# Optimization experiments

Hardware: AMD Instinct MI355X
Metric: run time of the kernel (lower is better)

## Reference

```python
import jax, jax.numpy as jnp
import numpy as np

EPS = 1e-6


def _mp_match(reps, att, kernel):
    """BiMPM multi-perspective match.
    reps: (B,L,D); att: (B,L,D) or (B,1,D); kernel: (M,D).
    Returns (B,L,1+M): [tanh(sum(reps*att)), tanh(sum_d reps*kernel_m*att)].
    """
    prod = reps * att                                   # (B,L,D)
    cos = jnp.tanh(jnp.sum(prod, axis=-1, keepdims=True))   # (B,L,1)
    mp = jnp.tanh(jnp.einsum('bld,md->blm', prod, kernel))  # (B,L,M)
    return jnp.concatenate([cos, mp], axis=-1)


def setup_inputs() -> dict:
    key = jax.random.key(0)
    ks = jax.random.split(key, 12)
    B, Llt, Lrt, D, M, A = 32, 128, 128, 512, 64, 128
    H = D // 2
    u = lambda k, shape: jax.random.uniform(k, shape, jnp.float32, -0.05, 0.05)  # keras 'uniform' init
    return {
        'reps_lt': jax.random.normal(ks[0], (B, Llt, D), jnp.float32),
        'h_lt_fw': jax.random.normal(ks[1], (B, H), jnp.float32),
        'h_lt_bw': jax.random.normal(ks[2], (B, H), jnp.float32),
        'reps_rt': jax.random.normal(ks[3], (B, Lrt, D), jnp.float32),
        'h_rt_fw': jax.random.normal(ks[4], (B, H), jnp.float32),
        'h_rt_bw': jax.random.normal(ks[5], (B, H), jnp.float32),
        'kernel_full': u(ks[6], (M, D)),
        'kernel_mpool': u(ks[7], (M, D)),
        'attn_w1': u(ks[8], (D, A)),
        'diag_w': u(ks[9], (A,)),
        'kernel_att': u(ks[10], (M, D)),
        'kernel_maxatt': u(ks[11], (M, D)),
    }


def reference(reps_lt, h_lt_fw, h_lt_bw, reps_rt, h_rt_fw, h_rt_bw,
              kernel_full, kernel_mpool, attn_w1, diag_w,
              kernel_att, kernel_maxatt):
    # ---- full match: each left timestep vs last BiLSTM state of right ----
    h_rt = jnp.concatenate([h_rt_fw, h_rt_bw], axis=-1)[:, None, :]  # (B,1,D)
    full = _mp_match(reps_lt, h_rt, kernel_full)                     # (B,Ll,1+M)

    # ---- max-pooling match ----
    # t[b,r,l,m] = tanh(sum_d R[b,r,d]*K[m,d]*L[b,l,d]); max over right positions r
    r_scaled = jnp.einsum('brd,md->brmd', reps_rt, kernel_mpool)     # (B,Lr,M,D)
    t = jnp.tanh(jnp.einsum('brmd,bld->brlm', r_scaled, reps_lt))    # (B,Lr,Ll,M)
    mpool = jnp.max(t, axis=1)                                       # (B,Ll,M)

    # ---- attentive match ----
    a_lt = jnp.tanh(reps_lt @ attn_w1) * diag_w                      # (B,Ll,A)
    a_rt = jnp.tanh(reps_rt @ attn_w1)                               # (B,Lr,A)
    scores = jnp.einsum('bla,bra->blr', a_lt, a_rt)                  # (B,Ll,Lr)
    probs = jax.nn.softmax(scores, axis=-1)
    att = jnp.einsum('blr,brd->bld', probs, reps_rt)                 # (B,Ll,D)
    attentive = _mp_match(reps_lt, att, kernel_att)                  # (B,Ll,1+M)

    # ---- max-attentive match ----
    num = jnp.einsum('bld,brd->blr', reps_lt, reps_rt)
    n_lt = jnp.sqrt(jnp.maximum(jnp.sum(reps_lt * reps_lt, -1), EPS))[:, :, None]
    n_rt = jnp.sqrt(jnp.maximum(jnp.sum(reps_rt * reps_rt, -1), EPS))[:, None, :]
    rel = num / n_rt / n_lt                                          # (B,Ll,Lr)
    idx = jnp.argmax(rel, axis=2)                                    # (B,Ll) int
    max_att = jnp.take_along_axis(reps_rt, idx[:, :, None], axis=1)  # (B,Ll,D)
    maxatt = _mp_match(reps_lt, max_att, kernel_maxatt)              # (B,Ll,1+M)

    return jnp.concatenate([full, mpool, attentive, maxatt], axis=-1)  # (B,Ll,3+4M)
```

## Files before the change

kernel.cpp:

```cpp
#include <hip/hip_runtime.h>
#include <hip/hip_bf16.h>
#include <math.h>
#include <stdint.h>

typedef __attribute__((ext_vector_type(8))) short short8;
typedef __attribute__((ext_vector_type(4))) float float4v;

#define DEV static __device__ __forceinline__

DEV float bflo(unsigned int u) { union { unsigned int i; float f; } v; v.i = u << 16; return v.f; }
DEV float bfhi(unsigned int u) { union { unsigned int i; float f; } v; v.i = u & 0xffff0000u; return v.f; }
DEV unsigned short f2bf(float f) {
    union { float f; unsigned int i; } v; v.f = f;
    unsigned int x = v.i;
    return (unsigned short)((x + 0x7fffu + ((x >> 16) & 1u)) >> 16);
}
DEV unsigned int pack2(float a, float b) { return (unsigned int)f2bf(a) | ((unsigned int)f2bf(b) << 16); }
#if __has_builtin(__builtin_amdgcn_cvt_pk_bf16_f32)
DEV unsigned int pack2_fast(float a, float b) {
    typedef __attribute__((ext_vector_type(2))) short short2v;
    short2v r = __builtin_amdgcn_cvt_pk_bf16_f32(a, b);
    union { short2v s; unsigned int u; } v; v.s = r; return v.u;
}
#else
DEV unsigned int pack2_fast(float a, float b) { return pack2(a, b); }
#endif
DEV void unpack8(uint4 u, float* f) {
    f[0]=bflo(u.x); f[1]=bfhi(u.x); f[2]=bflo(u.y); f[3]=bfhi(u.y);
    f[4]=bflo(u.z); f[5]=bfhi(u.z); f[6]=bflo(u.w); f[7]=bfhi(u.w);
}

DEV void async16(const unsigned short* g, unsigned short* l) {
    __builtin_amdgcn_global_load_lds(
        (const __attribute__((address_space(1))) unsigned int*)g,
        (__attribute__((address_space(3))) unsigned int*)l, 16, 0, 0);
}

__global__ __launch_bounds__(256) void prep_kernel(const float* __restrict__ lt,
                                                   const float* __restrict__ rt,
                                                   const float* __restrict__ kf,
                                                   const float* __restrict__ kmp,
                                                   const float* __restrict__ ka,
                                                   const float* __restrict__ km,
                                                   const float* __restrict__ w1,
                                                   unsigned short* __restrict__ ltb,
                                                   unsigned short* __restrict__ rtb,
                                                   unsigned short* __restrict__ kb,
                                                   unsigned short* __restrict__ w1t,
                                                   double* __restrict__ rsq) {
    __shared__ double ws2[2][2];
    __shared__ float tile[32][33];
    int bid = blockIdx.x, t = threadIdx.x;
    if (bid < 1024) {
        bool isRt = bid >= 512;
        int base = (isRt ? (bid - 512) : bid) * 8;
        int rl = t >> 7;
        int c  = t & 127;
        const float* srcb = isRt ? rt : lt;
        unsigned short* dstb = isRt ? rtb : ltb;
        #pragma unroll
        for (int p = 0; p < 4; ++p) {
            int row = base + p * 2 + rl;
            const float* src = srcb + (size_t)row * 512;
            float4 v = *(const float4*)(src + c * 4);
            ushort4 o;
            o.x = f2bf(v.x); o.y = f2bf(v.y); o.z = f2bf(v.z); o.w = f2bf(v.w);
            *(ushort4*)(dstb + (size_t)row * 512 + c * 4) = o;
            if (isRt) {
                double s = (double)v.x * v.x + (double)v.y * v.y
                         + (double)v.z * v.z + (double)v.w * v.w;
                #pragma unroll
                for (int off = 1; off < 64; off <<= 1) s += __shfl_xor(s, off, 64);
                if ((c & 63) == 0) ws2[rl][c >> 6] = s;
                __syncthreads();
                if (c == 0) rsq[row] = 1.0 / sqrt(ws2[rl][0] + ws2[rl][1]);
                __syncthreads();
            }
        }
    } else if (bid < 1152) {
        int kbk = bid - 1024;
        int ksel = kbk >> 5;
        const float* src = (ksel == 0) ? kf : (ksel == 1) ? kmp : (ksel == 2) ? ka : km;
        int off = (kbk & 31) * 1024 + t * 4;
        float4 v = *(const float4*)(src + off);
        ushort4 o;
        o.x = f2bf(v.x); o.y = f2bf(v.y); o.z = f2bf(v.z); o.w = f2bf(v.w);
        *(ushort4*)(kb + ksel * 32768 + off) = o;
    } else {
        int b2 = bid - 1152;
        int d0 = (b2 & 15) * 32, a0 = (b2 >> 4) * 32;
        int r = t >> 5, c = t & 31;
        #pragma unroll
        for (int i = 0; i < 32; i += 8)
            tile[r + i][c] = w1[(size_t)(d0 + r + i) * 128 + a0 + c];
        __syncthreads();
        #pragma unroll
        for (int i = 0; i < 32; i += 8)
            w1t[(size_t)(a0 + r + i) * 512 + d0 + c] = f2bf(tile[c][r + i]);
    }
}

__global__ __launch_bounds__(256, 3) void uber_kernel(
        const unsigned short* __restrict__ ltb,
        const unsigned short* __restrict__ rtb,
        const unsigned short* __restrict__ kmb,
        const unsigned short* __restrict__ w1t,
        const float* __restrict__ diag,
        unsigned short* __restrict__ a_all,
        const float* __restrict__ ltf,
        const float* __restrict__ rtf,
        const double* __restrict__ rsq,
        int* __restrict__ idxout,
        float* __restrict__ out) {
    __shared__ __align__(16) unsigned char smem[52224];
    int bx = blockIdx.x;
    int t = threadIdx.x;
    int wave = t >> 6, lane = t & 63;
    int q = lane >> 4, col = lane & 15, kq = q * 8;

    if (bx < 2048) {
        int xcd = bx & 7, jj = bx >> 3;
        int b = xcd * 4 + (jj >> 6);
        int m = jj & 63;
        unsigned short (*ltS)[72] = (unsigned short(*)[72])smem;
        unsigned short* rtL = (unsigned short*)(smem + 18432);
        float (*mx)[2] = (float(*)[2])(smem + 18432 + 32768);
        int wl = wave & 1, wr = wave >> 1;
        const unsigned short* ltp = ltb + (size_t)b * 65536;
        const unsigned short* rtp = rtb + (size_t)b * 65536;
        const unsigned short* kr = kmb + (size_t)m * 512;
        int srow = t >> 3, cg8 = t & 7, cg = cg8 * 8;
        int gsw = (cg8 ^ (srow & 7)) * 8;
        int wbase = (t & ~63) * 8;

        #pragma unroll
        for (int it = 0; it < 4; ++it)
            async16(rtp + (size_t)(it * 32 + srow) * 512 + gsw,
                    rtL + it * 2048 + wbase);
        uint4 pk = *(const uint4*)(kr + cg);
        uint4 plt[4];
        #pragma unroll
        for (int it = 0; it < 4; ++it)
            plt[it] = *(const uint4*)(ltp + (size_t)(it * 32 + srow) * 512 + cg);

        float4v acc[4][4] = {};
        for (int k0i = 0; k0i < 8; ++k0i) {
            float kf8[8]; unpack8(pk, kf8);
            #pragma unroll
            for (int it = 0; it < 4; ++it) {
                int row = it * 32 + srow;
                float lf[8]; unpack8(plt[it], lf);
                uint4 s;
                s.x = pack2_fast(lf[0] * kf8[0], lf[1] * kf8[1]);
                s.y = pack2_fast(lf[2] * kf8[2], lf[3] * kf8[3]);
                s.z = pack2_fast(lf[4] * kf8[4], lf[5] * kf8[5]);
                s.w = pack2_fast(lf[6] * kf8[6], lf[7] * kf8[7]);
                *(uint4*)&ltS[row][cg] = s;
            }
            __syncthreads();
            if (k0i < 7) {
                int k0n = (k0i + 1) * 64;
                int bofs = ((k0i + 1) & 1) * 8192;
                #pragma unroll
                for (int it = 0; it < 4; ++it)
                    async16(rtp + (size_t)(it * 32 + srow) * 512 + k0n + gsw,
                            rtL + bofs + it * 2048 + wbase);
                pk = *(const uint4*)(kr + k0n + cg);
                #pragma unroll
                for (int it = 0; it < 4; ++it)
                    plt[it] = *(const uint4*)(ltp + (size_t)(it * 32 + srow) * 512 + k0n + cg);
            }
            const unsigned short* rb = rtL + (k0i & 1) * 8192;
            #pragma unroll
            for (int kk = 0; kk < 64; kk += 32) {
                short8 af[4], bfr[4];
                #pragma unroll
                for (int i = 0; i < 4; ++i)
                    af[i] = *(const short8*)&ltS[wl * 64 + i * 16 + col][kk + kq];
                #pragma unroll
                for (int j = 0; j < 4; ++j) {
                    int row = wr * 64 + j * 16 + col;
                    int slot = ((kk >> 3) + q) ^ (row & 7);
                    bfr[j] = *(const short8*)&rb[row * 64 + slot * 8];
                }
                #pragma unroll
                for (int i = 0; i < 4; ++i)
                    #pragma unroll
                    for (int j = 0; j < 4; ++j)
                        acc[i][j] = __builtin_amdgcn_mfma_f32_16x16x32_bf16(af[i], bfr[j], acc[i][j], 0, 0, 0);
            }
            __syncthreads();
        }
        #pragma unroll
        for (int i = 0; i < 4; ++i)
            #pragma unroll
            for (int ii = 0; ii < 4; ++ii) {
                float v = fmaxf(fmaxf(acc[i][0][ii], acc[i][1][ii]), fmaxf(acc[i][2][ii], acc[i][3][ii]));
                #pragma unroll
                for (int off = 1; off < 16; off <<= 1) v = fmaxf(v, __shfl_xor(v, off, 64));
                if (col == 0) mx[wl * 64 + i * 16 + q * 4 + ii][wr] = v;
            }
        __syncthreads();
        if (t < 128)
            out[((size_t)(b * 128 + t)) * 259 + 65 + m] = tanhf(fmaxf(mx[t][0], mx[t][1]));

    } else if (bx < 2560) {
        int idA = bx - 2048;
        int xcd = idA & 7, jj = idA >> 3;
        int b = xcd * 4 + (jj >> 4);
        int L0 = (jj & 15) * 8;
        float* ltS = (float*)smem;
        float* buf = (float*)(smem + 16384);
        double* dvs = (double*)(smem + 49152);
        float* wv1 = (float*)(smem + 49152 + 128);
        float* wv2 = wv1 + 16;
        int* wi1 = (int*)(wv2 + 16);
        int* wi2 = wi1 + 16;
        int* candi = wi2 + 16;
        {
            int row = t >> 5, c0 = (t & 31) * 16;
            const float* src = ltf + ((size_t)(b * 128 + L0 + row)) * 512 + c0;
            #pragma unroll
            for (int i = 0; i < 4; ++i)
                *(float4*)&ltS[row * 512 + c0 + i * 4] = *(const float4*)(src + i * 4);
        }
        int lg = t >> 7;
        int rg = (t >> 2) & 31;
        int ds = t & 3;
        float acc[4][4] = {{0.f}};
        for (int p = 0; p < 8; ++p) {
            __syncthreads();
            {
                int row = t >> 1, c0 = (t & 1) * 32;
                const float* src = rtf + ((size_t)(b * 128 + row)) * 512 + p * 64 + c0;
                float f[32];
                #pragma unroll
                for (int i = 0; i < 8; ++i)
                    *(float4*)&f[i * 4] = *(const float4*)(src + i * 4);
                int base = row * 64;
                #pragma unroll
                for (int gg = 0; gg < 4; ++gg) {
                    int g = (t & 1) * 4 + gg;
                    int o = ((g ^ (row & 7)) * 8);
                    #pragma unroll
                    for (int k = 0; k < 8; ++k) buf[base + o + k] = f[gg * 8 + k];
                }
            }
            __syncthreads();
            #pragma unroll
            for (int sub = 0; sub < 2; ++sub) {
                int dloc = ds * 16 + sub * 8;
                int dglob = p * 64 + dloc;
                float a[4][8];
                #pragma unroll
                for (int i = 0; i < 4; ++i)
                    #pragma unroll
                    for (int k = 0; k < 8; ++k) a[i][k] = ltS[(lg * 4 + i) * 512 + dglob + k];
                int g = dloc >> 3;
                #pragma unroll
                for (int j = 0; j < 4; ++j) {
                    int r = rg + j * 32;
                    const float* rp = &buf[r * 64 + ((g ^ (r & 7)) * 8)];
                    float rv[8];
                    #pragma unroll
                    for (int k = 0; k < 8; ++k) rv[k] = rp[k];
                    #pragma unroll
                    for (int i = 0; i < 4; ++i)
                        #pragma unroll
                        for (int k = 0; k < 8; ++k)
                            acc[i][j] = fmaf(a[i][k], rv[k], acc[i][j]);
                }
            }
        }
        #pragma unroll
        for (int i = 0; i < 4; ++i)
            #pragma unroll
            for (int j = 0; j < 4; ++j) {
                acc[i][j] += __shfl_xor(acc[i][j], 1, 64);
                acc[i][j] += __shfl_xor(acc[i][j], 2, 64);
            }
        float v1[4], v2[4]; int i1[4], i2[4];
        #pragma unroll
        for (int i = 0; i < 4; ++i) {
            v1[i] = -3.0e38f; v2[i] = -3.0e38f; i1[i] = 0; i2[i] = 1;
            #pragma unroll
            for (int j = 0; j < 4; ++j) {
                int r = rg + j * 32;
                float s = acc[i][j] * (float)rsq[b * 128 + r];
                if (s > v1[i]) { v2[i] = v1[i]; i2[i] = i1[i]; v1[i] = s; i1[i] = r; }
                else if (s > v2[i]) { v2[i] = s; i2[i] = r; }
            }
        }
        #pragma unroll
        for (int off = 4; off < 64; off <<= 1) {
            #pragma unroll
            for (int i = 0; i < 4; ++i) {
                float u1 = __shfl_xor(v1[i], off, 64); int j1 = __shfl_xor(i1[i], off, 64);
                float u2 = __shfl_xor(v2[i], off, 64); int j2 = __shfl_xor(i2[i], off, 64);
                if (u1 > v1[i]) {
                    float ov = v1[i]; int oi = i1[i];
                    v1[i] = u1; i1[i] = j1;
                    if (u2 > ov) { v2[i] = u2; i2[i] = j2; } else { v2[i] = ov; i2[i] = oi; }
                } else if (u1 > v2[i]) { v2[i] = u1; i2[i] = j1; }
            }
        }
        if (lane == 0) {
            #pragma unroll
            for (int i = 0; i < 4; ++i) {
                int l = lg * 4 + i, h = wave & 1;
                wv1[l * 2 + h] = v1[i]; wi1[l * 2 + h] = i1[i];
                wv2[l * 2 + h] = v2[i]; wi2[l * 2 + h] = i2[i];
            }
        }
        __syncthreads();
        if (t < 8) {
            float a1 = wv1[t * 2], a2 = wv2[t * 2]; int ai1 = wi1[t * 2], ai2 = wi2[t * 2];
            float b1 = wv1[t * 2 + 1], b2 = wv2[t * 2 + 1]; int bi1 = wi1[t * 2 + 1], bi2 = wi2[t * 2 + 1];
            int ri1, ri2;
            if (b1 > a1) {
                ri1 = bi1;
                if (b2 > a1) { ri2 = bi2; } else { ri2 = ai1; }
            } else {
                ri1 = ai1;
                if (b1 > a2) { ri2 = bi1; } else { ri2 = ai2; }
            }
            candi[t * 2] = ri1; candi[t * 2 + 1] = ri2;
            (void)a2; (void)b2; (void)ai2; (void)bi2;
        }
        __syncthreads();
        {
            int dotid = t >> 4;
            int sub = t & 15;
            int l = dotid >> 1, c = dotid & 1;
            int r = candi[l * 2 + c];
            const float* lrow = ltf + ((size_t)(b * 128 + L0 + l)) * 512;
            const float* rrow = rtf + ((size_t)(b * 128 + r)) * 512;
            double s = 0.0;
            #pragma unroll 8
            for (int k = 0; k < 32; ++k) {
                int d = sub * 32 + k;
                s = fma((double)lrow[d], (double)rrow[d], s);
            }
            #pragma unroll
            for (int off = 1; off < 16; off <<= 1) s += __shfl_xor(s, off, 64);
            if (sub == 0) dvs[l * 2 + c] = s * rsq[b * 128 + r];
        }
        __syncthreads();
        if (t < 8) {
            int ia = candi[t * 2], ib = candi[t * 2 + 1];
            double va = dvs[t * 2], vb = dvs[t * 2 + 1];
            int res = (vb > va || (vb == va && ib < ia)) ? ib : ia;
            idxout[b * 128 + L0 + t] = res;
        }

    } else {
        int R0 = (bx - 2560) * 32;
        unsigned short (*aS)[72] = (unsigned short(*)[72])smem;
        unsigned short (*bS)[72] = (unsigned short(*)[72])(smem + 4608);
        float* diagS = (float*)(smem + 4608 + 18432);
        int wl = wave & 1, wr = wave >> 1;
        if (t < 128) diagS[t] = diag[t];
        const unsigned short* src = (R0 < 4096) ? (ltb + (size_t)R0 * 512) : (rtb + (size_t)(R0 - 4096) * 512);
        float4v acc[4] = {};
        for (int k0 = 0; k0 < 512; k0 += 64) {
            {
                int row = t >> 3, cg = (t & 7) * 8;
                *(uint4*)&aS[row][cg] = *(const uint4*)(src + (size_t)row * 512 + k0 + cg);
            }
            #pragma unroll
            for (int it = 0; it < 4; ++it) {
                int id = it * 256 + t;
                int row = id >> 3, cg = (id & 7) * 8;
                *(uint4*)&bS[row][cg] = *(const uint4*)(w1t + (size_t)row * 512 + k0 + cg);
            }
            __syncthreads();
            #pragma unroll
            for (int kk = 0; kk < 64; kk += 32) {
                short8 af = *(const short8*)&aS[wl * 16 + col][kk + kq];
                #pragma unroll
                for (int j = 0; j < 4; ++j) {
                    short8 bf = *(const short8*)&bS[wr * 64 + j * 16 + col][kk + kq];
                    acc[j] = __builtin_amdgcn_mfma_f32_16x16x32_bf16(af, bf, acc[j], 0, 0, 0);
                }
            }
            __syncthreads();
        }
        bool isLt = (R0 < 4096);
        #pragma unroll
        for (int j = 0; j < 4; ++j)
            #pragma unroll
            for (int ii = 0; ii < 4; ++ii) {
                int rowl = wl * 16 + q * 4 + ii;
                int n = wr * 64 + j * 16 + col;
                float v = tanhf(acc[j][ii]);
                if (isLt) v *= diagS[n];
                a_all[((size_t)(R0 + rowl)) * 128 + n] = f2bf(v);
            }
    }
}

__global__ __launch_bounds__(512, 4) void tail_kernel(
        const unsigned short* __restrict__ a_all,
        const unsigned short* __restrict__ rtb,
        const float* __restrict__ ltf,
        const unsigned short* __restrict__ kb,
        const float* __restrict__ hfw,
        const float* __restrict__ hbw,
        const int* __restrict__ idxp,
        float* __restrict__ out) {
    __shared__ __align__(16) unsigned char smem[81664];
    int bx = blockIdx.x;
    int t = threadIdx.x;
    int wave = t >> 6, lane = t & 63;
    int q = lane >> 4, col = lane & 15, kq = q * 8;

    if (bx < 256) {
        int b = bx & 31, lg = bx >> 5;
        int L0 = lg * 16;
        unsigned short (*altS)[136]  = (unsigned short(*)[136])(smem);
        unsigned short (*artS)[136]  = (unsigned short(*)[136])(smem + 4352);
        unsigned short (*rtS)[512]   = (unsigned short(*)[512])(smem + 39168);
        unsigned short (*prodsF)[520]= (unsigned short(*)[520])(smem + 55552);
        float (*P)[132]  = (float(*)[132])(smem + 72192);
        float (*pmax)[8] = (float(*)[8])(smem + 80640);
        float (*psum)[8] = (float(*)[8])(smem + 81152);
        const unsigned short* kb_att = kb + 2 * 32768;

        if (t < 256) {
            int row = t >> 4, c0 = (t & 15) * 8;
            *(uint4*)&altS[row][c0] = *(const uint4*)(a_all + ((size_t)(b * 128 + L0 + row)) * 128 + c0);
        }
        {
            int row = t >> 2, c0 = (t & 3) * 32;
            const unsigned short* src = a_all + ((size_t)(4096 + b * 128 + row)) * 128 + c0;
            #pragma unroll
            for (int i = 0; i < 4; ++i)
                *(uint4*)&artS[row][c0 + i * 8] = *(const uint4*)(src + i * 8);
        }
        __syncthreads();

        float4v acc = {};
        #pragma unroll
        for (int kk = 0; kk < 128; kk += 32) {
            short8 af = *(const short8*)&altS[col][kk + kq];
            short8 bf = *(const short8*)&artS[wave * 16 + col][kk + kq];
            acc = __builtin_amdgcn_mfma_f32_16x16x32_bf16(af, bf, acc, 0, 0, 0);
        }
        float m4[4], p4[4];
        #pragma unroll
        for (int ii = 0; ii < 4; ++ii) {
            float v = acc[ii];
            #pragma unroll
            for (int off = 1; off < 16; off <<= 1) v = fmaxf(v, __shfl_xor(v, off, 64));
            m4[ii] = v;
        }
        if (col == 0) {
            #pragma unroll
            for (int ii = 0; ii < 4; ++ii) pmax[q * 4 + ii][wave] = m4[ii];
        }
        __syncthreads();
        #pragma unroll
        for (int ii = 0; ii < 4; ++ii) {
            float M = pmax[q * 4 + ii][0];
            #pragma unroll
            for (int w = 1; w < 8; ++w) M = fmaxf(M, pmax[q * 4 + ii][w]);
            p4[ii] = expf(acc[ii] - M);
            float s = p4[ii];
            #pragma unroll
            for (int off = 1; off < 16; off <<= 1) s += __shfl_xor(s, off, 64);
            m4[ii] = s;
        }
        if (col == 0) {
            #pragma unroll
            for (int ii = 0; ii < 4; ++ii) psum[q * 4 + ii][wave] = m4[ii];
        }
        __syncthreads();
        #pragma unroll
        for (int ii = 0; ii < 4; ++ii) {
            float S = psum[q * 4 + ii][0] + psum[q * 4 + ii][1] + psum[q * 4 + ii][2] + psum[q * 4 + ii][3]
                    + psum[q * 4 + ii][4] + psum[q * 4 + ii][5] + psum[q * 4 + ii][6] + psum[q * 4 + ii][7];
            P[q * 4 + ii][wave * 16 + col] = p4[ii] / S;
        }

        int l = t >> 5, cd = t & 31;
        float a8[2][8] = {{0.f}};
        for (int rcb = 0; rcb < 128; rcb += 16) {
            __syncthreads();
            {
                int row = t >> 5, c0 = (t & 31) * 16;
                const unsigned short* src = rtb + ((size_t)(b * 128 + rcb + row)) * 512 + c0;
                *(uint4*)&rtS[row][c0] = *(const uint4*)src;
                *(uint4*)&rtS[row][c0 + 8] = *(const uint4*)(src + 8);
            }
            __syncthreads();
            for (int rr = 0; rr < 16; ++rr) {
                float pr = P[l][rcb + rr];
                #pragma unroll
                for (int pass = 0; pass < 2; ++pass) {
                    uint4 u = *(const uint4*)&rtS[rr][pass * 256 + cd * 8];
                    float f[8]; unpack8(u, f);
                    #pragma unroll
                    for (int k = 0; k < 8; ++k) a8[pass][k] += pr * f[k];
                }
            }
        }

        int grow = b * 128 + L0 + l;
        const float* ltrow = ltf + (size_t)grow * 512;
        float csum = 0.f;
        #pragma unroll
        for (int pass = 0; pass < 2; ++pass) {
            int d0 = pass * 256 + cd * 8;
            float lf[8];
            *(float4*)&lf[0] = *(const float4*)(ltrow + d0);
            *(float4*)&lf[4] = *(const float4*)(ltrow + d0 + 4);
            float pf[8];
            #pragma unroll
            for (int k = 0; k < 8; ++k) { pf[k] = lf[k] * a8[pass][k]; csum += pf[k]; }
            uint4 o;
            o.x = pack2(pf[0], pf[1]); o.y = pack2(pf[2], pf[3]);
            o.z = pack2(pf[4], pf[5]); o.w = pack2(pf[6], pf[7]);
            *(uint4*)&prodsF[l][d0] = o;
        }
        #pragma unroll
        for (int off = 1; off < 32; off <<= 1) csum += __shfl_xor(csum, off, 64);
        if (cd == 0) out[(size_t)grow * 259 + 129] = tanhf(csum);

        unsigned short* Ks = &artS[0][0];
        float* red = (float*)&rtS[0][0];
        for (int half = 0; half < 2; ++half) {
            __syncthreads();
            {
                int row = t >> 4, c0 = (t & 15) * 32;
                const unsigned short* src = kb_att + ((size_t)(half * 32 + row)) * 512 + c0;
                #pragma unroll
                for (int i = 0; i < 4; ++i)
                    *(uint4*)&Ks[row * 520 + c0 + i * 8] = *(const uint4*)(src + i * 8);
            }
            __syncthreads();
            float4v pacc[2] = {};
            #pragma unroll
            for (int kk = 0; kk < 64; kk += 32) {
                short8 af = *(const short8*)&prodsF[col][wave * 64 + kk + kq];
                #pragma unroll
                for (int j = 0; j < 2; ++j) {
                    short8 bf = *(const short8*)&Ks[(j * 16 + col) * 520 + wave * 64 + kk + kq];
                    pacc[j] = __builtin_amdgcn_mfma_f32_16x16x32_bf16(af, bf, pacc[j], 0, 0, 0);
                }
            }
            #pragma unroll
            for (int j = 0; j < 2; ++j)
                #pragma unroll
                for (int ii = 0; ii < 4; ++ii)
                    red[((wave * 2 + j) * 16 + q * 4 + ii) * 16 + col] = pacc[j][ii];
            __syncthreads();
            {
                int ll = t >> 5, jm = t & 31;
                int j = jm >> 4, mc = jm & 15;
                float s = 0.f;
                #pragma unroll
                for (int w = 0; w < 8; ++w) s += red[((w * 2 + j) * 16 + ll) * 16 + mc];
                out[((size_t)(b * 128 + L0 + ll)) * 259 + 130 + half * 32 + jm] = tanhf(s);
            }
        }

    } else {
        int idB = bx - 256;
        int lg = idB & 7, b = (idB >> 3) & 31;
        int mode = (idB >> 8) ? 2 : 0;
        int L0 = lg * 16;
        unsigned short (*prods)[520] = (unsigned short(*)[520])smem;
        unsigned short* Ks = (unsigned short*)(smem + 16640);
        float* red = (float*)(smem + 49920);
        const unsigned short* Kp = kb + (size_t)((mode == 0) ? 0 : 3 * 32768);
        int obase = (mode == 0) ? 0 : 194;

        if (t < 256) {
            int l = t >> 4, c = t & 15;
            int grow = b * 128 + L0 + l;
            const float* ltrow = ltf + (size_t)grow * 512;
            const unsigned short* avrow = 0;
            if (mode == 2) avrow = rtb + ((size_t)(b * 128 + idxp[grow])) * 512;
            float csum = 0.f;
            #pragma unroll
            for (int pass = 0; pass < 4; ++pass) {
                int d0 = pass * 128 + c * 8;
                float lf[8], af[8], pf[8];
                *(float4*)&lf[0] = *(const float4*)(ltrow + d0);
                *(float4*)&lf[4] = *(const float4*)(ltrow + d0 + 4);
                if (mode == 0) {
                    const float* h = (d0 < 256) ? (hfw + b * 256 + d0) : (hbw + b * 256 + d0 - 256);
                    *(float4*)&af[0] = *(const float4*)h;
                    *(float4*)&af[4] = *(const float4*)(h + 4);
                } else {
                    uint4 av = *(const uint4*)(avrow + d0);
                    unpack8(av, af);
                }
                #pragma unroll
                for (int k = 0; k < 8; ++k) { pf[k] = lf[k] * af[k]; csum += pf[k]; }
                uint4 o;
                o.x = pack2(pf[0], pf[1]); o.y = pack2(pf[2], pf[3]);
                o.z = pack2(pf[4], pf[5]); o.w = pack2(pf[6], pf[7]);
                *(uint4*)&prods[l][d0] = o;
            }
            #pragma unroll
            for (int off = 1; off < 16; off <<= 1) csum += __shfl_xor(csum, off, 64);
            if (c == 0) out[(size_t)grow * 259 + obase] = tanhf(csum);
        }
        for (int half = 0; half < 2; ++half) {
            {
                int row = t >> 4, c0 = (t & 15) * 32;
                const unsigned short* src = Kp + ((size_t)(half * 32 + row)) * 512 + c0;
                #pragma unroll
                for (int i = 0; i < 4; ++i)
                    *(uint4*)&Ks[row * 520 + c0 + i * 8] = *(const uint4*)(src + i * 8);
            }
            __syncthreads();
            float4v acc2[2] = {};
            #pragma unroll
            for (int kk = 0; kk < 64; kk += 32) {
                short8 af = *(const short8*)&prods[col][wave * 64 + kk + kq];
                #pragma unroll
                for (int j = 0; j < 2; ++j) {
                    short8 bf = *(const short8*)&Ks[(j * 16 + col) * 520 + wave * 64 + kk + kq];
                    acc2[j] = __builtin_amdgcn_mfma_f32_16x16x32_bf16(af, bf, acc2[j], 0, 0, 0);
                }
            }
            #pragma unroll
            for (int j = 0; j < 2; ++j)
                #pragma unroll
                for (int ii = 0; ii < 4; ++ii)
                    red[((wave * 2 + j) * 16 + q * 4 + ii) * 16 + col] = acc2[j][ii];
            __syncthreads();
            {
                int ll = t >> 5, jm = t & 31;
                int j = jm >> 4, mc = jm & 15;
                float s = 0.f;
                #pragma unroll
                for (int w = 0; w < 8; ++w) s += red[((w * 2 + j) * 16 + ll) * 16 + mc];
                out[((size_t)(b * 128 + L0 + ll)) * 259 + obase + 1 + half * 32 + jm] = tanhf(s);
            }
            __syncthreads();
        }
    }
}

extern "C" void kernel_launch(void* const* d_in, const int* in_sizes, int n_in,
                              void* d_out, int out_size, void* d_ws, size_t ws_size,
                              hipStream_t stream) {
    const float* lt  = (const float*)d_in[0];
    const float* rt  = (const float*)d_in[3];
    const float* hfw = (const float*)d_in[4];
    const float* hbw = (const float*)d_in[5];
    const float* kf  = (const float*)d_in[6];
    const float* kmp = (const float*)d_in[7];
    const float* w1  = (const float*)d_in[8];
    const float* dia = (const float*)d_in[9];
    const float* ka  = (const float*)d_in[10];
    const float* km  = (const float*)d_in[11];
    float* out = (float*)d_out;

    char* wsb = (char*)d_ws;
    unsigned short* ltb16 = (unsigned short*)(wsb);
    unsigned short* rtb16 = (unsigned short*)(wsb + 4194304);
    unsigned short* kb16  = (unsigned short*)(wsb + 8388608);
    unsigned short* w1t   = (unsigned short*)(wsb + 8650752);
    unsigned short* a_all = (unsigned short*)(wsb + 8781824);
    double*         rsq   = (double*)(wsb + 15073280);
    int*            idx   = (int*)(wsb + 15106048);

    prep_kernel<<<1216, 256, 0, stream>>>(lt, rt, kf, kmp, ka, km, w1, ltb16, rtb16, kb16, w1t, rsq);
    uber_kernel<<<2816, 256, 0, stream>>>(ltb16, rtb16, kb16 + 32768, w1t, dia, a_all,
                                          lt, rt, rsq, idx, out);
    tail_kernel<<<768, 512, 0, stream>>>(a_all, rtb16, lt, kb16, hfw, hbw, idx, out);
}
```

Measured before the change: 188.9 us.

## Load max-pool MFMA operands directly from global memory, dropping LDS staging

The max-pooling match block no longer stages the left (kernel-scaled) and right tiles through shared memory with async global-to-LDS copies and double buffering. Each lane now reads its MFMA fragments straight from global memory, scaling the left fragment by the kernel row in registers, and all intra-loop barriers are removed. This cuts LDS traffic and synchronisation but makes each wave re-read operands other waves also use. It depends on L2/cache hits and gives up the explicit prefetch overlap, and the global fragment reads are strided by row.

```diff
diff --git a/kernel.cpp b/kernel.cpp
--- a/kernel.cpp
+++ b/kernel.cpp
@@ -28,12 +28,6 @@
 DEV void unpack8(uint4 u, float* f) {
     f[0]=bflo(u.x); f[1]=bfhi(u.x); f[2]=bflo(u.y); f[3]=bfhi(u.y);
     f[4]=bflo(u.z); f[5]=bfhi(u.z); f[6]=bflo(u.w); f[7]=bfhi(u.w);
-}
-
-DEV void async16(const unsigned short* g, unsigned short* l) {
-    __builtin_amdgcn_global_load_lds(
-        (const __attribute__((address_space(1))) unsigned int*)g,
-        (__attribute__((address_space(3))) unsigned int*)l, 16, 0, 0);
 }
 
 __global__ __launch_bounds__(256) void prep_kernel(const float* __restrict__ lt,
@@ -122,66 +116,38 @@
         int xcd = bx & 7, jj = bx >> 3;
         int b = xcd * 4 + (jj >> 6);
         int m = jj & 63;
-        unsigned short (*ltS)[72] = (unsigned short(*)[72])smem;
-        unsigned short* rtL = (unsigned short*)(smem + 18432);
-        float (*mx)[2] = (float(*)[2])(smem + 18432 + 32768);
+        float (*mx)[2] = (float(*)[2])smem;
         int wl = wave & 1, wr = wave >> 1;
-        const unsigned short* ltp = ltb + (size_t)b * 65536;
-        const unsigned short* rtp = rtb + (size_t)b * 65536;
-        const unsigned short* kr = kmb + (size_t)m * 512;
-        int srow = t >> 3, cg8 = t & 7, cg = cg8 * 8;
-        int gsw = (cg8 ^ (srow & 7)) * 8;
-        int wbase = (t & ~63) * 8;
-
-        #pragma unroll
-        for (int it = 0; it < 4; ++it)
-            async16(rtp + (size_t)(it * 32 + srow) * 512 + gsw,
-                    rtL + it * 2048 + wbase);
-        uint4 pk = *(const uint4*)(kr + cg);
-        uint4 plt[4];
-        #pragma unroll
-        for (int it = 0; it < 4; ++it)
-            plt[it] = *(const uint4*)(ltp + (size_t)(it * 32 + srow) * 512 + cg);
+
+        const unsigned short* pK = kmb + (size_t)m * 512 + kq;
+        const unsigned short* pA[4];
+        const unsigned short* pB[4];
+        #pragma unroll
+        for (int i = 0; i < 4; ++i) {
+            pA[i] = ltb + ((size_t)(b * 128 + wl * 64 + i * 16 + col)) * 512 + kq;
+            pB[i] = rtb + ((size_t)(b * 128 + wr * 64 + i * 16 + col)) * 512 + kq;
+        }
 
         float4v acc[4][4] = {};
+        #pragma unroll
         for (int k0i = 0; k0i < 8; ++k0i) {
-            float kf8[8]; unpack8(pk, kf8);
-            #pragma unroll
-            for (int it = 0; it < 4; ++it) {
-                int row = it * 32 + srow;
-                float lf[8]; unpack8(plt[it], lf);
-                uint4 s;
-                s.x = pack2_fast(lf[0] * kf8[0], lf[1] * kf8[1]);
-                s.y = pack2_fast(lf[2] * kf8[2], lf[3] * kf8[3]);
-                s.z = pack2_fast(lf[4] * kf8[4], lf[5] * kf8[5]);
-                s.w = pack2_fast(lf[6] * kf8[6], lf[7] * kf8[7]);
-                *(uint4*)&ltS[row][cg] = s;
-            }
-            __syncthreads();
-            if (k0i < 7) {
-                int k0n = (k0i + 1) * 64;
-                int bofs = ((k0i + 1) & 1) * 8192;
-                #pragma unroll
-                for (int it = 0; it < 4; ++it)
-                    async16(rtp + (size_t)(it * 32 + srow) * 512 + k0n + gsw,
-                            rtL + bofs + it * 2048 + wbase);
-                pk = *(const uint4*)(kr + k0n + cg);
-                #pragma unroll
-                for (int it = 0; it < 4; ++it)
-                    plt[it] = *(const uint4*)(ltp + (size_t)(it * 32 + srow) * 512 + k0n + cg);
-            }
-            const unsigned short* rb = rtL + (k0i & 1) * 8192;
             #pragma unroll
             for (int kk = 0; kk < 64; kk += 32) {
+                int off = k0i * 64 + kk;
+                uint4 ku = *(const uint4*)(pK + off);
+                float kf8[8]; unpack8(ku, kf8);
                 short8 af[4], bfr[4];
                 #pragma unroll
-                for (int i = 0; i < 4; ++i)
-                    af[i] = *(const short8*)&ltS[wl * 64 + i * 16 + col][kk + kq];
-                #pragma unroll
-                for (int j = 0; j < 4; ++j) {
-                    int row = wr * 64 + j * 16 + col;
-                    int slot = ((kk >> 3) + q) ^ (row & 7);
-                    bfr[j] = *(const short8*)&rb[row * 64 + slot * 8];
+                for (int i = 0; i < 4; ++i) {
+                    uint4 au = *(const uint4*)(pA[i] + off);
+                    float lf[8]; unpack8(au, lf);
+                    uint4 s;
+                    s.x = pack2_fast(lf[0] * kf8[0], lf[1] * kf8[1]);
+                    s.y = pack2_fast(lf[2] * kf8[2], lf[3] * kf8[3]);
+                    s.z = pack2_fast(lf[4] * kf8[4], lf[5] * kf8[5]);
+                    s.w = pack2_fast(lf[6] * kf8[6], lf[7] * kf8[7]);
+                    af[i] = *(short8*)&s;
+                    bfr[i] = *(const short8*)(pB[i] + off);
                 }
                 #pragma unroll
                 for (int i = 0; i < 4; ++i)
@@ -189,7 +155,6 @@
                     for (int j = 0; j < 4; ++j)
                         acc[i][j] = __builtin_amdgcn_mfma_f32_16x16x32_bf16(af[i], bfr[j], acc[i][j], 0, 0, 0);
             }
-            __syncthreads();
         }
         #pragma unroll
         for (int i = 0; i < 4; ++i)
```

Result: slower. 262.9 us (+39.2%).
